# Optimization experiments

Measured on AMD Instinct MI355X. Metric: run time of the kernel, lower is better.

Reference implementation:

```python
import jax, jax.numpy as jnp
import numpy as np

N_NODES = 100000
N_EDGES = 3200000
STATE_DIM = 128
ACTION_DIM = 8


def _w(key, shape, scale=0.05):
    return (jax.random.normal(key, shape, dtype=jnp.float32) * scale)


def setup_inputs() -> dict:
    key = jax.random.key(0)
    ks = jax.random.split(key, 24)
    x = jax.random.normal(ks[0], (N_NODES, STATE_DIM), dtype=jnp.float32)
    edge_index = jax.random.randint(ks[1], (2, N_EDGES), 0, N_NODES, dtype=jnp.int64)
    inp = {
        "x": x,
        "edge_index": edge_index,
        # GCN layers (weights stored [in, out] so forward is x @ W + b)
        "W1": _w(ks[2], (STATE_DIM, 128)), "b1": jnp.zeros((128,), jnp.float32),
        "W2": _w(ks[3], (128, 128)),       "b2": jnp.zeros((128,), jnp.float32),
        "W3": _w(ks[4], (128, 64)),        "b3": jnp.zeros((64,), jnp.float32),
        # actor MLP 64->128->64->ACTION_DIM + softmax
        "Wa1": _w(ks[5], (64, 128)),  "ba1": jnp.zeros((128,), jnp.float32),
        "Wa2": _w(ks[6], (128, 64)),  "ba2": jnp.zeros((64,), jnp.float32),
        "Wa3": _w(ks[7], (64, ACTION_DIM)), "ba3": jnp.zeros((ACTION_DIM,), jnp.float32),
        # critic MLP 64->128->64->1
        "Wc1": _w(ks[8], (64, 128)),  "bc1": jnp.zeros((128,), jnp.float32),
        "Wc2": _w(ks[9], (128, 64)),  "bc2": jnp.zeros((64,), jnp.float32),
        "Wc3": _w(ks[10], (64, 1)),   "bc3": jnp.zeros((1,), jnp.float32),
    }
    return inp


def _gcn_conv(x, W, b, src, dst, norm):
    # GCNConv: D^{-1/2} (A + I) D^{-1/2} X W + b  (self loops already in src/dst)
    h = x @ W                                   # [N, out]
    msg = h[src] * norm[:, None]                # gather + per-edge scale
    agg = jax.ops.segment_sum(msg, dst, num_segments=N_NODES)
    return agg + b


def reference(x, edge_index,
              W1, b1, W2, b2, W3, b3,
              Wa1, ba1, Wa2, ba2, Wa3, ba3,
              Wc1, bc1, Wc2, bc2, Wc3, bc3):
    loop = jnp.arange(N_NODES, dtype=edge_index.dtype)
    src = jnp.concatenate([edge_index[0], loop])
    dst = jnp.concatenate([edge_index[1], loop])
    deg = jax.ops.segment_sum(jnp.ones_like(dst, dtype=x.dtype), dst,
                              num_segments=N_NODES)
    dinv = jax.lax.rsqrt(deg)                   # deg >= 1 via self loops
    norm = dinv[src] * dinv[dst]                # [E+N]

    # forward_gnn (dropout is identity in eval mode)
    h = jax.nn.relu(_gcn_conv(x, W1, b1, src, dst, norm))
    h = jax.nn.relu(_gcn_conv(h, W2, b2, src, dst, norm))
    h = _gcn_conv(h, W3, b3, src, dst, norm)    # [N, 64]

    a = jax.nn.relu(h @ Wa1 + ba1)
    a = jax.nn.relu(a @ Wa2 + ba2)
    probs = jax.nn.softmax(a @ Wa3 + ba3, axis=-1)   # [N, ACTION_DIM]

    c = jax.nn.relu(h @ Wc1 + bc1)
    c = jax.nn.relu(c @ Wc2 + bc2)
    values = c @ Wc3 + bc3                      # [N, 1]

    return jnp.concatenate([probs, values], axis=-1)  # [N, ACTION_DIM+1]
```

## Files before the change

kernel.cpp:

```cpp
#include <hip/hip_runtime.h>
#include <hip/hip_bf16.h>
#include <math.h>


#define WS_ALIGN(x) (((x) + 255) & ~(size_t)255)

constexpr int RNG  = 64;
constexpr int NRG  = 1563;
constexpr int NB   = 1024;
constexpr int CHK  = 16;

constexpr float S_FP8     = 64.0f;
constexpr float S_FP8_INV = 1.0f / 64.0f;

using bf16x8 = __attribute__((ext_vector_type(8))) short;
using f32x4  = __attribute__((ext_vector_type(4))) float;
using f32x2  = __attribute__((ext_vector_type(2))) float;

__device__ __forceinline__ float b2f(unsigned short u) {
    return __uint_as_float(((unsigned int)u) << 16);
}
__device__ __forceinline__ unsigned short f2b(float f) {
    __hip_bfloat16 hb = __float2bfloat16(f);
    return *(unsigned short*)&hb;
}
__device__ __forceinline__ unsigned char f2fp8(float f) {
    return (unsigned char)(__builtin_amdgcn_cvt_pk_fp8_f32(f, f, 0, false) & 0xff);
}
__device__ __forceinline__ int pad8(int v) { return (v + 7) & ~7; }

__device__ __forceinline__ void acc8(uint2 u, f32x2& a01, f32x2& a23,
                                     f32x2& a45, f32x2& a67) {
    a01 += __builtin_amdgcn_cvt_pk_f32_fp8((int)u.x, false);
    a23 += __builtin_amdgcn_cvt_pk_f32_fp8((int)u.x, true);
    a45 += __builtin_amdgcn_cvt_pk_f32_fp8((int)u.y, false);
    a67 += __builtin_amdgcn_cvt_pk_f32_fp8((int)u.y, true);
}


__global__ __launch_bounds__(256) void bucket_count_k(
    const int* __restrict__ dst, int* __restrict__ bcnt, int E) {
    __shared__ int c64[RNG];
    int b = blockIdx.x, t = threadIdx.x;
    if (t < RNG) c64[t] = 0;
    __syncthreads();
    int ec = (E + NB - 1) / NB;
    int e0 = b * ec, e1 = min(E, e0 + ec);
    for (int e = e0 + t; e < e1; e += 256) {
        int d = __builtin_nontemporal_load(dst + e);
        atomicAdd(&c64[d / NRG], 1);
    }
    __syncthreads();
    if (t < RNG) bcnt[t * NB + b] = c64[t];
}

__global__ __launch_bounds__(256) void rsum_k(
    const int* __restrict__ bcnt, int* __restrict__ base, int* __restrict__ rtot) {
    __shared__ int s[256];
    int r = blockIdx.x, t = threadIdx.x;
    const int* row = bcnt + (size_t)r * NB;
    int v[4], loc = 0;
#pragma unroll
    for (int j = 0; j < 4; j++) { v[j] = row[t * 4 + j]; loc += v[j]; }
    s[t] = loc;
    __syncthreads();
    for (int d = 1; d < 256; d <<= 1) {
        int x = (t >= d) ? s[t - d] : 0;
        __syncthreads();
        s[t] += x;
        __syncthreads();
    }
    int run = s[t] - loc;
    int* bp = base + (size_t)r * NB + t * 4;
#pragma unroll
    for (int j = 0; j < 4; j++) { bp[j] = run; run += v[j]; }
    if (t == 255) rtot[r] = s[255];
}

__global__ void rstart_k(const int* __restrict__ rtot, int* __restrict__ bstart, int E) {
    if (threadIdx.x == 0) {
        int run = 0;
        for (int r = 0; r < RNG; r++) { bstart[r] = run; run += rtot[r]; }
        bstart[RNG] = run;
    }
}

__global__ __launch_bounds__(256) void bucket_scatter_k(
    const int* __restrict__ src, const int* __restrict__ dst,
    const int* __restrict__ base, const int* __restrict__ bstart,
    unsigned* __restrict__ bucket, int E) {
    __shared__ int cur[RNG];
    int b = blockIdx.x, t = threadIdx.x;
    if (t < RNG) cur[t] = bstart[t] + base[(size_t)t * NB + b];
    __syncthreads();
    int ec = (E + NB - 1) / NB;
    int e0 = b * ec, e1 = min(E, e0 + ec);
    for (int e = e0 + t; e < e1; e += 256) {
        int d = __builtin_nontemporal_load(dst + e);
        int sv = __builtin_nontemporal_load(src + e);
        int r = d / NRG;
        int pos = atomicAdd(&cur[r], 1);
        bucket[pos] = ((unsigned)(d - r * NRG) << 17) | (unsigned)sv;
    }
}

__global__ __launch_bounds__(256) void hist_bucket_k(
    const unsigned* __restrict__ bucket, const int* __restrict__ bstart,
    int* __restrict__ hist) {
    __shared__ int h[NRG];
    int b = blockIdx.x, r = b & 63, c2 = b >> 6, t = threadIdx.x;
    for (int i = t; i < NRG; i += 256) h[i] = 0;
    int s0 = bstart[r], s1 = bstart[r + 1];
    int ec = (s1 - s0 + CHK - 1) / CHK;
    int e0 = s0 + c2 * ec, e1 = min(s1, e0 + ec);
    __syncthreads();
    for (int e = e0 + t; e < e1; e += 256) {
        unsigned v = __builtin_nontemporal_load(bucket + e);
        atomicAdd(&h[v >> 17], 1);
    }
    __syncthreads();
    int* out = hist + ((size_t)r * CHK + c2) * NRG;
    for (int i = t; i < NRG; i += 256) out[i] = h[i];
}

__global__ void sum_hist_dinv_k(const int* __restrict__ hist, int* __restrict__ cnt,
                                float* __restrict__ dinv, int N) {
    int i = blockIdx.x * 256 + threadIdx.x;
    if (i >= N) return;
    int r = i / NRG, li = i - r * NRG;
    const int* hp = hist + ((size_t)r * CHK) * NRG + li;
    int s = 0;
#pragma unroll
    for (int c = 0; c < CHK; c++) s += hp[(size_t)c * NRG];
    cnt[i] = s;
    dinv[i] = rsqrtf((float)s + 1.0f);
}

__global__ void chunk_sum_k(const int* __restrict__ cnt, int* __restrict__ bsum, int n) {
    __shared__ int sd[256];
    int t = threadIdx.x;
    int i = blockIdx.x * 256 + t;
    sd[t] = (i < n) ? pad8(cnt[i]) : 0;
    __syncthreads();
    for (int d = 128; d > 0; d >>= 1) {
        if (t < d) sd[t] += sd[t + d];
        __syncthreads();
    }
    if (t == 0) bsum[blockIdx.x] = sd[0];
}

__global__ void scan_mid_k(const int* __restrict__ bsum, int* __restrict__ boff,
                           int nb, int* __restrict__ rowptr, int N) {
    __shared__ int s[512];
    int t = threadIdx.x;
    s[t] = (t < nb) ? bsum[t] : 0;
    __syncthreads();
    if (t == 0) {
        int run = 0;
        for (int i = 0; i < nb; i++) { int v = s[i]; s[i] = run; run += v; }
        rowptr[N] = run;
    }
    __syncthreads();
    if (t < nb) boff[t] = s[t];
}

__global__ void scan_off_pad_k(const int* __restrict__ cnt, const int* __restrict__ boff,
                               int* __restrict__ rowptr, int* __restrict__ hist,
                               int* __restrict__ col, int N) {
    __shared__ int s[256];
    int t = threadIdx.x;
    int i = blockIdx.x * 256 + t;
    int cv = (i < N) ? cnt[i] : 0;
    int v = pad8(cv);
    if (i >= N) v = 0;
    s[t] = v;
    __syncthreads();
    for (int d = 1; d < 256; d <<= 1) {
        int x = (t >= d) ? s[t - d] : 0;
        __syncthreads();
        s[t] += x;
        __syncthreads();
    }
    if (i < N) {
        int rp = s[t] - v + boff[blockIdx.x];
        rowptr[i] = rp;
        int r = i / NRG, li = i - r * NRG;
        int* hp = hist + ((size_t)r * CHK) * NRG + li;
        int run = rp;
#pragma unroll
        for (int c = 0; c < CHK; c++) {
            int hv = hp[(size_t)c * NRG];
            hp[(size_t)c * NRG] = run;
            run += hv;
        }
        for (int e = rp + cv; e < rp + v; e++) col[e] = N;
    }
}

__global__ __launch_bounds__(256) void fill2_k(
    const unsigned* __restrict__ bucket, const int* __restrict__ bstart,
    const int* __restrict__ hist, int* __restrict__ col) {
    __shared__ int cur[NRG];
    int b = blockIdx.x, r = b & 63, c2 = b >> 6, t = threadIdx.x;
    const int* hp = hist + ((size_t)r * CHK + c2) * NRG;
    for (int i = t; i < NRG; i += 256) cur[i] = hp[i];
    int s0 = bstart[r], s1 = bstart[r + 1];
    int ec = (s1 - s0 + CHK - 1) / CHK;
    int e0 = s0 + c2 * ec, e1 = min(s1, e0 + ec);
    __syncthreads();
    for (int e = e0 + t; e < e1; e += 256) {
        unsigned v = __builtin_nontemporal_load(bucket + e);
        int slot = atomicAdd(&cur[v >> 17], 1);
        col[slot] = (int)(v & 0x1FFFFu);
    }
}


__global__ __launch_bounds__(256) void prep_w_k(
    const float* __restrict__ W1, const float* __restrict__ W2,
    const float* __restrict__ W3, const float* __restrict__ Wa1,
    const float* __restrict__ Wc1, const float* __restrict__ Wa2,
    const float* __restrict__ Wc2, unsigned short* __restrict__ wt) {
    int i = blockIdx.x * 256 + threadIdx.x;
    const float* W; int off, K, OUT;
    if (i < 16384)      { W = W1;  off = 0;     K = 128; OUT = 128; }
    else if (i < 32768) { W = W2;  off = 16384; K = 128; OUT = 128; }
    else if (i < 40960) { W = W3;  off = 32768; K = 128; OUT = 64; }
    else if (i < 49152) { W = Wa1; off = 40960; K = 64;  OUT = 128; }
    else if (i < 57344) { W = Wc1; off = 49152; K = 64;  OUT = 128; }
    else if (i < 65536) { W = Wa2; off = 57344; K = 128; OUT = 64; }
    else                { W = Wc2; off = 65536; K = 128; OUT = 64; }
    int j = i - off, k = j / OUT, n = j - k * OUT;
    wt[off + n * K + k] = f2b(W[j]);
}


template <int K, int OUT, int EPI, bool AF32>
__global__ __launch_bounds__(256) void gemm2_k(
    const void* __restrict__ Xv, int ldx, const unsigned short* __restrict__ Wt,
    const float* __restrict__ sb, const float* __restrict__ w3b,
    const float* __restrict__ b3, void* __restrict__ Yv, int N, int NT) {
    constexpr int LDK = K + 8;
    __shared__ __align__(16) unsigned short Bs[OUT * LDK];
    __shared__ __align__(16) unsigned short As[64 * LDK];
    int t = threadIdx.x;

    for (int g = t; g < OUT * (K / 8); g += 256) {
        int r = g / (K / 8), q = g - r * (K / 8);
        *(uint4*)&Bs[r * LDK + q * 8] = *(const uint4*)(Wt + r * K + q * 8);
    }

    int wv = t >> 6, lane = t & 63;
    int lm = lane & 15, lq = lane >> 4;
    constexpr int CT = OUT / 16;

    for (int tile = blockIdx.x; tile < NT; tile += gridDim.x) {
        int rowBase = tile * 64;

        if constexpr (AF32) {
            const float* X = (const float*)Xv;
            for (int g = t; g < 64 * (K / 8); g += 256) {
                int r = g / (K / 8), q = g - r * (K / 8);
                int gr = rowBase + r;
                unsigned short us[8];
                if (gr < N) {
                    float4 v0 = *(const float4*)(X + (size_t)gr * ldx + q * 8);
                    float4 v1 = *(const float4*)(X + (size_t)gr * ldx + q * 8 + 4);
                    us[0] = f2b(v0.x); us[1] = f2b(v0.y); us[2] = f2b(v0.z); us[3] = f2b(v0.w);
                    us[4] = f2b(v1.x); us[5] = f2b(v1.y); us[6] = f2b(v1.z); us[7] = f2b(v1.w);
                } else {
#pragma unroll
                    for (int j = 0; j < 8; j++) us[j] = 0;
                }
                *(uint4*)&As[r * LDK + q * 8] = *(uint4*)us;
            }
        } else {
            const unsigned short* X = (const unsigned short*)Xv;
            for (int g = t; g < 64 * (K / 8); g += 256) {
                int r = g / (K / 8), q = g - r * (K / 8);
                int gr = rowBase + r;
                uint4 v = make_uint4(0, 0, 0, 0);
                if (gr < N) v = *(const uint4*)(X + (size_t)gr * ldx + q * 8);
                *(uint4*)&As[r * LDK + q * 8] = v;
            }
        }
        __syncthreads();

        f32x4 acc[CT];
#pragma unroll
        for (int c = 0; c < CT; c++) acc[c] = (f32x4){0.f, 0.f, 0.f, 0.f};

        const unsigned short* arow = &As[(wv * 16 + lm) * LDK + lq * 8];
#pragma unroll
        for (int kt = 0; kt < K / 32; kt++) {
            bf16x8 a = *(const bf16x8*)(arow + kt * 32);
#pragma unroll
            for (int c = 0; c < CT; c++) {
                bf16x8 b = *(const bf16x8*)&Bs[(c * 16 + lm) * LDK + kt * 32 + lq * 8];
                acc[c] = __builtin_amdgcn_mfma_f32_16x16x32_bf16(a, b, acc[c], 0, 0, 0);
            }
        }

        int r0 = rowBase + wv * 16 + lq * 4;
        if constexpr (EPI == 0) {
#pragma unroll
            for (int r = 0; r < 4; r++) {
                int gr = r0 + r;
                float scale = (gr < N) ? sb[gr] * S_FP8 : 0.f;
#pragma unroll
                for (int c = 0; c < CT; c++) {
                    int colg = c * 16 + lm;
                    ((unsigned char*)Yv)[(size_t)gr * OUT + colg] = f2fp8(acc[c][r] * scale);
                }
            }
        }
        __syncthreads();
    }
}


template <bool RELU>
__global__ __launch_bounds__(256) void agg128_k(
    const unsigned char* __restrict__ H,
    const int* __restrict__ rowptr, const int* __restrict__ col,
    const float* __restrict__ dinv, const float* __restrict__ bias,
    unsigned short* __restrict__ Y, int N, int Ecap) {
    int tid = threadIdx.x;
    int node = blockIdx.x * 4 + (tid >> 6);
    if (node >= N) return;
    int lane = tid & 63;
    int grp = lane >> 4;
    int li8 = (lane & 15) * 8;

    f32x2 a01 = {0.f, 0.f}, a23 = {0.f, 0.f}, a45 = {0.f, 0.f}, a67 = {0.f, 0.f};
    if (grp == 0) {
        uint2 u = *(const uint2*)(H + (size_t)node * 128 + li8);
        acc8(u, a01, a23, a45, a67);
    }

    int start = rowptr[node], end = rowptr[node + 1];
    for (int e0 = start; e0 < end; e0 += 64) {
        int cv = col[min(e0 + lane, Ecap - 1)];
        int quads = min(64, end - e0) >> 2;
        for (int q = 0; q < quads; q += 2) {
            int s0 = __shfl(cv, 4 * q + grp, 64);
            int s1 = __shfl(cv, 4 * q + 4 + grp, 64);
            uint2 u0 = *(const uint2*)(H + (size_t)s0 * 128 + li8);
            uint2 u1 = *(const uint2*)(H + (size_t)s1 * 128 + li8);
            acc8(u0, a01, a23, a45, a67);
            acc8(u1, a01, a23, a45, a67);
        }
    }

#pragma unroll
    for (int w = 16; w < 64; w <<= 1) {
        a01[0] += __shfl_xor(a01[0], w, 64); a01[1] += __shfl_xor(a01[1], w, 64);
        a23[0] += __shfl_xor(a23[0], w, 64); a23[1] += __shfl_xor(a23[1], w, 64);
        a45[0] += __shfl_xor(a45[0], w, 64); a45[1] += __shfl_xor(a45[1], w, 64);
        a67[0] += __shfl_xor(a67[0], w, 64); a67[1] += __shfl_xor(a67[1], w, 64);
    }

    if (grp == 0) {
        float dv = dinv[node] * S_FP8_INV;
        float4 b0 = *(const float4*)(bias + li8);
        float4 b1 = *(const float4*)(bias + li8 + 4);
        float o0 = a01[0] * dv + b0.x, o1 = a01[1] * dv + b0.y;
        float o2 = a23[0] * dv + b0.z, o3 = a23[1] * dv + b0.w;
        float o4 = a45[0] * dv + b1.x, o5 = a45[1] * dv + b1.y;
        float o6 = a67[0] * dv + b1.z, o7 = a67[1] * dv + b1.w;
        if (RELU) {
            o0 = fmaxf(o0, 0.f); o1 = fmaxf(o1, 0.f); o2 = fmaxf(o2, 0.f); o3 = fmaxf(o3, 0.f);
            o4 = fmaxf(o4, 0.f); o5 = fmaxf(o5, 0.f); o6 = fmaxf(o6, 0.f); o7 = fmaxf(o7, 0.f);
        }
        unsigned short us[8] = {f2b(o0), f2b(o1), f2b(o2), f2b(o3),
                                f2b(o4), f2b(o5), f2b(o6), f2b(o7)};
        *(uint4*)(Y + (size_t)node * 128 + li8) = *(uint4*)us;
    }
}

__global__ __launch_bounds__(256) void agg64_k(
    const unsigned char* __restrict__ H,
    const int* __restrict__ rowptr, const int* __restrict__ col,
    const float* __restrict__ dinv, const float* __restrict__ bias,
    unsigned short* __restrict__ Y, int N, int Ecap) {
    int tid = threadIdx.x;
    int node = blockIdx.x * 4 + (tid >> 6);
    if (node >= N) return;
    int lane = tid & 63;
    int grp = lane >> 3;
    int li8 = (lane & 7) * 8;

    f32x2 a01 = {0.f, 0.f}, a23 = {0.f, 0.f}, a45 = {0.f, 0.f}, a67 = {0.f, 0.f};
    if (grp == 0) {
        uint2 u = *(const uint2*)(H + (size_t)node * 64 + li8);
        acc8(u, a01, a23, a45, a67);
    }

    int start = rowptr[node], end = rowptr[node + 1];
    for (int e0 = start; e0 < end; e0 += 64) {
        int cv = col[min(e0 + lane, Ecap - 1)];
        int octs = min(64, end - e0) >> 3;
        int o = 0;
        for (; o + 2 <= octs; o += 2) {
            int s0 = __shfl(cv, 8 * o + grp, 64);
            int s1 = __shfl(cv, 8 * o + 8 + grp, 64);
            uint2 u0 = *(const uint2*)(H + (size_t)s0 * 64 + li8);
            uint2 u1 = *(const uint2*)(H + (size_t)s1 * 64 + li8);
            acc8(u0, a01, a23, a45, a67);
            acc8(u1, a01, a23, a45, a67);
        }
        if (o < octs) {
            int s0 = __shfl(cv, 8 * o + grp, 64);
            uint2 u0 = *(const uint2*)(H + (size_t)s0 * 64 + li8);
            acc8(u0, a01, a23, a45, a67);
        }
    }

#pragma unroll
    for (int w = 8; w < 64; w <<= 1) {
        a01[0] += __shfl_xor(a01[0], w, 64); a01[1] += __shfl_xor(a01[1], w, 64);
        a23[0] += __shfl_xor(a23[0], w, 64); a23[1] += __shfl_xor(a23[1], w, 64);
        a45[0] += __shfl_xor(a45[0], w, 64); a45[1] += __shfl_xor(a45[1], w, 64);
        a67[0] += __shfl_xor(a67[0], w, 64); a67[1] += __shfl_xor(a67[1], w, 64);
    }

    if (grp == 0) {
        float dv = dinv[node] * S_FP8_INV;
        float4 b0 = *(const float4*)(bias + li8);
        float4 b1 = *(const float4*)(bias + li8 + 4);
        unsigned short us[8] = {
            f2b(a01[0] * dv + b0.x), f2b(a01[1] * dv + b0.y),
            f2b(a23[0] * dv + b0.z), f2b(a23[1] * dv + b0.w),
            f2b(a45[0] * dv + b1.x), f2b(a45[1] * dv + b1.y),
            f2b(a67[0] * dv + b1.z), f2b(a67[1] * dv + b1.w)};
        *(uint4*)(Y + (size_t)node * 64 + li8) = *(uint4*)us;
    }
}


template <int EPI>
__global__ __launch_bounds__(256) void heads_k(
    const unsigned short* __restrict__ h3,
    const unsigned short* __restrict__ W1t,
    const float* __restrict__ b1v,
    const unsigned short* __restrict__ W2t,
    const float* __restrict__ b2v,
    const float* __restrict__ w3,
    const float* __restrict__ b3v,
    float* __restrict__ out, int N, int NT) {
    constexpr int LD64 = 72, LD128 = 136;
    __shared__ __align__(16) unsigned short Bs1[128 * LD64];
    __shared__ __align__(16) unsigned short Bs2[64 * LD128];
    __shared__ __align__(16) unsigned short As[4 * 16 * LD64];
    __shared__ __align__(16) unsigned short A1[4 * 16 * LD128];
    int t = threadIdx.x, wv = t >> 6, lane = t & 63;
    int lm = lane & 15, lq = lane >> 4;

    for (int g = t; g < 128 * 8; g += 256) {
        int r = g >> 3, q = g & 7;
        *(uint4*)&Bs1[r * LD64 + q * 8] = *(const uint4*)(W1t + r * 64 + q * 8);
    }
    for (int g = t; g < 64 * 16; g += 256) {
        int r = g >> 4, q = g & 15;
        *(uint4*)&Bs2[r * LD128 + q * 8] = *(const uint4*)(W2t + r * 128 + q * 8);
    }
    __syncthreads();

    unsigned short* Asw = &As[wv * 16 * LD64];
    unsigned short* A1w = &A1[wv * 16 * LD128];

    for (int tile = blockIdx.x; tile < NT; tile += gridDim.x) {
        int rowBase = tile * 64 + wv * 16;

        for (int g = lane; g < 16 * 8; g += 64) {
            int r = g >> 3, q = g & 7;
            int gr = rowBase + r;
            uint4 v = make_uint4(0, 0, 0, 0);
            if (gr < N) v = *(const uint4*)(h3 + (size_t)gr * 64 + q * 8);
            *(uint4*)&Asw[r * LD64 + q * 8] = v;
        }

        f32x4 acc1[8];
#pragma unroll
        for (int c = 0; c < 8; c++) acc1[c] = (f32x4){0.f, 0.f, 0.f, 0.f};
        const unsigned short* arow = &Asw[lm * LD64 + lq * 8];
#pragma unroll
        for (int kt = 0; kt < 2; kt++) {
            bf16x8 a = *(const bf16x8*)(arow + kt * 32);
#pragma unroll
            for (int c = 0; c < 8; c++) {
                bf16x8 b = *(const bf16x8*)&Bs1[(c * 16 + lm) * LD64 + kt * 32 + lq * 8];
                acc1[c] = __builtin_amdgcn_mfma_f32_16x16x32_bf16(a, b, acc1[c], 0, 0, 0);
            }
        }
#pragma unroll
        for (int r = 0; r < 4; r++) {
            int lr = lq * 4 + r;
#pragma unroll
            for (int c = 0; c < 8; c++) {
                int colg = c * 16 + lm;
                float v = fmaxf(acc1[c][r] + b1v[colg], 0.f);
                A1w[lr * LD128 + colg] = f2b(v);
            }
        }

        f32x4 acc[4];
#pragma unroll
        for (int c = 0; c < 4; c++) acc[c] = (f32x4){0.f, 0.f, 0.f, 0.f};
        const unsigned short* arow2 = &A1w[lm * LD128 + lq * 8];
#pragma unroll
        for (int kt = 0; kt < 4; kt++) {
            bf16x8 a = *(const bf16x8*)(arow2 + kt * 32);
#pragma unroll
            for (int c = 0; c < 4; c++) {
                bf16x8 b = *(const bf16x8*)&Bs2[(c * 16 + lm) * LD128 + kt * 32 + lq * 8];
                acc[c] = __builtin_amdgcn_mfma_f32_16x16x32_bf16(a, b, acc[c], 0, 0, 0);
            }
        }

        int r0 = rowBase + lq * 4;
        if constexpr (EPI == 2) {
            float l[4][8];
#pragma unroll
            for (int r = 0; r < 4; r++)
#pragma unroll
                for (int a = 0; a < 8; a++) l[r][a] = 0.f;
#pragma unroll
            for (int c = 0; c < 4; c++) {
                int colg = c * 16 + lm;
#pragma unroll
                for (int r = 0; r < 4; r++) {
                    float v = fmaxf(acc[c][r] + b2v[colg], 0.f);
#pragma unroll
                    for (int a = 0; a < 8; a++)
                        l[r][a] = fmaf(v, w3[colg * 8 + a], l[r][a]);
                }
            }
#pragma unroll
            for (int w = 1; w < 16; w <<= 1)
#pragma unroll
                for (int r = 0; r < 4; r++)
#pragma unroll
                    for (int a = 0; a < 8; a++)
                        l[r][a] += __shfl_xor(l[r][a], w, 64);
            if (lm < 8) {
#pragma unroll
                for (int r = 0; r < 4; r++) {
                    int gr = r0 + r;
                    if (gr < N) {
                        float lg[8], m = -1e30f;
#pragma unroll
                        for (int a = 0; a < 8; a++) { lg[a] = l[r][a] + b3v[a]; m = fmaxf(m, lg[a]); }
                        float sum = 0.f;
#pragma unroll
                        for (int a = 0; a < 8; a++) { lg[a] = expf(lg[a] - m); sum += lg[a]; }
                        out[(size_t)gr * 9 + lm] = lg[lm] / sum;
                    }
                }
            }
        } else {
            float lv[4] = {0.f, 0.f, 0.f, 0.f};
#pragma unroll
            for (int c = 0; c < 4; c++) {
                int colg = c * 16 + lm;
#pragma unroll
                for (int r = 0; r < 4; r++) {
                    float v = fmaxf(acc[c][r] + b2v[colg], 0.f);
                    lv[r] = fmaf(v, w3[colg], lv[r]);
                }
            }
#pragma unroll
            for (int w = 1; w < 16; w <<= 1)
#pragma unroll
                for (int r = 0; r < 4; r++) lv[r] += __shfl_xor(lv[r], w, 64);
            if (lm == 0) {
#pragma unroll
                for (int r = 0; r < 4; r++) {
                    int gr = r0 + r;
                    if (gr < N) out[(size_t)gr * 9 + 8] = lv[r] + b3v[0];
                }
            }
        }
    }
}


extern "C" void kernel_launch(void* const* d_in, const int* in_sizes, int n_in,
                              void* d_out, int out_size, void* d_ws, size_t ws_size,
                              hipStream_t stream) {
    const float* x   = (const float*)d_in[0];
    const int*   ei  = (const int*)d_in[1];
    const float* W1  = (const float*)d_in[2];  const float* b1  = (const float*)d_in[3];
    const float* W2  = (const float*)d_in[4];  const float* b2  = (const float*)d_in[5];
    const float* W3  = (const float*)d_in[6];  const float* b3  = (const float*)d_in[7];
    const float* Wa1 = (const float*)d_in[8];  const float* ba1 = (const float*)d_in[9];
    const float* Wa2 = (const float*)d_in[10]; const float* ba2 = (const float*)d_in[11];
    const float* Wa3 = (const float*)d_in[12]; const float* ba3 = (const float*)d_in[13];
    const float* Wc1 = (const float*)d_in[14]; const float* bc1 = (const float*)d_in[15];
    const float* Wc2 = (const float*)d_in[16]; const float* bc2 = (const float*)d_in[17];
    const float* Wc3 = (const float*)d_in[18]; const float* bc3 = (const float*)d_in[19];
    float* out = (float*)d_out;

    const int N = in_sizes[0] / 128;
    const int E = in_sizes[1] / 2;
    const int* src = ei;
    const int* dst = ei + E;
    const int Ecap = E + 8 * N;
    const int Npad = ((N + 63) / 64) * 64;
    const int NT   = (N + 63) / 64;

    size_t off = 0;
    auto take = [&](size_t bytes) { size_t o = off; off = WS_ALIGN(off + bytes); return o; };
    char* ws = (char*)d_ws;
    unsigned short* h3     = (unsigned short*)(ws + take((size_t)N * 64 * 2));
    unsigned short* h      = (unsigned short*)(ws + take((size_t)N * 128 * 2));
    unsigned char*  hpr8   = (unsigned char*) (ws + take((size_t)(Npad + 64) * 128));
    int*            col    = (int*)(ws + take((size_t)Ecap * 4));
    unsigned short* wt     = (unsigned short*)(ws + take(73728 * 2));
    float* dinv   = (float*)(ws + take((size_t)(N + 64) * 4));
    int*   cnt    = (int*)  (ws + take((size_t)N * 4));
    int*   rowptr = (int*)  (ws + take((size_t)(N + 1) * 4));
    int*   bcnt   = (int*)  (ws + take((size_t)RNG * NB * 4));
    int*   base   = (int*)  (ws + take((size_t)RNG * NB * 4));
    int*   rtot   = (int*)  (ws + take(RNG * 4));
    int*   bstart = (int*)  (ws + take((RNG + 1) * 4));
    int*   bsum   = (int*)  (ws + take(512 * 4));
    int*   boff   = (int*)  (ws + take(512 * 4));
    unsigned* bucket = (unsigned*)h;
    int* hist = (int*)h3;
    (void)ws_size; (void)n_in; (void)out_size;

    const int nb  = (N + 255) / 256;
    const int gN  = (N + 255) / 256;
    const int GG  = 512;

    prep_w_k<<<288, 256, 0, stream>>>(W1, W2, W3, Wa1, Wc1, Wa2, Wc2, wt);
    const unsigned short* W1t  = wt;
    const unsigned short* W2t  = wt + 16384;
    const unsigned short* W3t  = wt + 32768;
    const unsigned short* Wh1t = wt + 40960;
    const unsigned short* Wa2t = wt + 57344;
    const unsigned short* Wc2t = wt + 65536;

    bucket_count_k<<<NB, 256, 0, stream>>>(dst, bcnt, E);
    rsum_k<<<RNG, 256, 0, stream>>>(bcnt, base, rtot);
    rstart_k<<<1, 64, 0, stream>>>(rtot, bstart, E);
    bucket_scatter_k<<<NB, 256, 0, stream>>>(src, dst, base, bstart, bucket, E);
    hist_bucket_k<<<RNG * CHK, 256, 0, stream>>>(bucket, bstart, hist);
    sum_hist_dinv_k<<<gN, 256, 0, stream>>>(hist, cnt, dinv, N);
    chunk_sum_k<<<nb, 256, 0, stream>>>(cnt, bsum, N);
    scan_mid_k<<<1, 512, 0, stream>>>(bsum, boff, nb, rowptr, N);
    scan_off_pad_k<<<nb, 256, 0, stream>>>(cnt, boff, rowptr, hist, col, N);
    fill2_k<<<RNG * CHK, 256, 0, stream>>>(bucket, bstart, hist, col);

    gemm2_k<128, 128, 0, true><<<GG, 256, 0, stream>>>(
        x, 128, W1t, dinv, nullptr, nullptr, hpr8, N, NT);
    agg128_k<true><<<(N + 3) / 4, 256, 0, stream>>>(hpr8, rowptr, col, dinv, b1, h, N, Ecap);
    gemm2_k<128, 128, 0, false><<<GG, 256, 0, stream>>>(
        h, 128, W2t, dinv, nullptr, nullptr, hpr8, N, NT);
    agg128_k<true><<<(N + 3) / 4, 256, 0, stream>>>(hpr8, rowptr, col, dinv, b2, h, N, Ecap);
    gemm2_k<128, 64, 0, false><<<GG, 256, 0, stream>>>(
        h, 128, W3t, dinv, nullptr, nullptr, hpr8, N, NT);
    agg64_k<<<(N + 3) / 4, 256, 0, stream>>>(hpr8, rowptr, col, dinv, b3, h3, N, Ecap);

    heads_k<2><<<GG, 256, 0, stream>>>(h3, Wh1t, ba1, Wa2t, ba2, Wa3, ba3, out, N, NT);
    heads_k<3><<<GG, 256, 0, stream>>>(h3, Wh1t + 128 * 64, bc1, Wc2t, bc2, Wc3, bc3, out, N, NT);
}
```

Before: 482.7 us.

## Fuse scan kernels, merge actor/critic heads, and retune GEMM grid sizes

Folds the chunk-sum into the degree/dinv kernel and replaces the single-block mid scan by having each scan block reduce the preceding block sums itself, removing two launches. The actor and critic head kernels are merged into one kernel that loads the h3 tile once, and it now reads weights directly from global memory instead of staging them in LDS. Grid sizes for the GEMM kernels and the heads kernel are raised. The tradeoffs are redundant prefix reductions over bsum in every scan block and uncached global weight reads in the heads kernel.

```diff
diff --git a/kernel.cpp b/kernel.cpp
--- a/kernel.cpp
+++ b/kernel.cpp
@@ -123,24 +123,22 @@
     for (int i = t; i < NRG; i += 256) out[i] = h[i];
 }
 
-__global__ void sum_hist_dinv_k(const int* __restrict__ hist, int* __restrict__ cnt,
-                                float* __restrict__ dinv, int N) {
-    int i = blockIdx.x * 256 + threadIdx.x;
-    if (i >= N) return;
-    int r = i / NRG, li = i - r * NRG;
-    const int* hp = hist + ((size_t)r * CHK) * NRG + li;
-    int s = 0;
-#pragma unroll
-    for (int c = 0; c < CHK; c++) s += hp[(size_t)c * NRG];
-    cnt[i] = s;
-    dinv[i] = rsqrtf((float)s + 1.0f);
-}
-
-__global__ void chunk_sum_k(const int* __restrict__ cnt, int* __restrict__ bsum, int n) {
+__global__ __launch_bounds__(256) void sum_hist_dinv_k(
+    const int* __restrict__ hist, int* __restrict__ cnt,
+    float* __restrict__ dinv, int* __restrict__ bsum, int N) {
     __shared__ int sd[256];
     int t = threadIdx.x;
     int i = blockIdx.x * 256 + t;
-    sd[t] = (i < n) ? pad8(cnt[i]) : 0;
+    int s = 0;
+    if (i < N) {
+        int r = i / NRG, li = i - r * NRG;
+        const int* hp = hist + ((size_t)r * CHK) * NRG + li;
+#pragma unroll
+        for (int c = 0; c < CHK; c++) s += hp[(size_t)c * NRG];
+        cnt[i] = s;
+        dinv[i] = rsqrtf((float)s + 1.0f);
+    }
+    sd[t] = (i < N) ? pad8(s) : 0;
     __syncthreads();
     for (int d = 128; d > 0; d >>= 1) {
         if (t < d) sd[t] += sd[t + d];
@@ -149,27 +147,24 @@
     if (t == 0) bsum[blockIdx.x] = sd[0];
 }
 
-__global__ void scan_mid_k(const int* __restrict__ bsum, int* __restrict__ boff,
-                           int nb, int* __restrict__ rowptr, int N) {
-    __shared__ int s[512];
-    int t = threadIdx.x;
-    s[t] = (t < nb) ? bsum[t] : 0;
-    __syncthreads();
-    if (t == 0) {
-        int run = 0;
-        for (int i = 0; i < nb; i++) { int v = s[i]; s[i] = run; run += v; }
-        rowptr[N] = run;
-    }
-    __syncthreads();
-    if (t < nb) boff[t] = s[t];
-}
-
-__global__ void scan_off_pad_k(const int* __restrict__ cnt, const int* __restrict__ boff,
+__global__ void scan_off_pad_k(const int* __restrict__ cnt, const int* __restrict__ bsum,
                                int* __restrict__ rowptr, int* __restrict__ hist,
                                int* __restrict__ col, int N) {
     __shared__ int s[256];
-    int t = threadIdx.x;
-    int i = blockIdx.x * 256 + t;
+    int t = threadIdx.x, b = blockIdx.x;
+
+    int part = 0;
+    for (int j = t; j < b; j += 256) part += bsum[j];
+    s[t] = part;
+    __syncthreads();
+    for (int d = 128; d > 0; d >>= 1) {
+        if (t < d) s[t] += s[t + d];
+        __syncthreads();
+    }
+    int boffv = s[0];
+    __syncthreads();
+
+    int i = b * 256 + t;
     int cv = (i < N) ? cnt[i] : 0;
     int v = pad8(cv);
     if (i >= N) v = 0;
@@ -181,8 +176,9 @@
         s[t] += x;
         __syncthreads();
     }
+    if (b == (int)gridDim.x - 1 && t == 255) rowptr[N] = boffv + s[255];
     if (i < N) {
-        int rp = s[t] - v + boff[blockIdx.x];
+        int rp = s[t] - v + boffv;
         rowptr[i] = rp;
         int r = i / NRG, li = i - r * NRG;
         int* hp = hist + ((size_t)r * CHK) * NRG + li;
@@ -438,34 +434,22 @@
 }
 
 
-template <int EPI>
-__global__ __launch_bounds__(256) void heads_k(
+__global__ __launch_bounds__(256) void headsAC_k(
     const unsigned short* __restrict__ h3,
-    const unsigned short* __restrict__ W1t,
-    const float* __restrict__ b1v,
-    const unsigned short* __restrict__ W2t,
-    const float* __restrict__ b2v,
-    const float* __restrict__ w3,
-    const float* __restrict__ b3v,
+    const unsigned short* __restrict__ Wh1t,
+    const float* __restrict__ ba1, const float* __restrict__ bc1,
+    const unsigned short* __restrict__ Wa2t,
+    const float* __restrict__ ba2,
+    const unsigned short* __restrict__ Wc2t,
+    const float* __restrict__ bc2,
+    const float* __restrict__ Wa3, const float* __restrict__ ba3,
+    const float* __restrict__ Wc3, const float* __restrict__ bc3,
     float* __restrict__ out, int N, int NT) {
     constexpr int LD64 = 72, LD128 = 136;
-    __shared__ __align__(16) unsigned short Bs1[128 * LD64];
-    __shared__ __align__(16) unsigned short Bs2[64 * LD128];
     __shared__ __align__(16) unsigned short As[4 * 16 * LD64];
     __shared__ __align__(16) unsigned short A1[4 * 16 * LD128];
     int t = threadIdx.x, wv = t >> 6, lane = t & 63;
     int lm = lane & 15, lq = lane >> 4;
-
-    for (int g = t; g < 128 * 8; g += 256) {
-        int r = g >> 3, q = g & 7;
-        *(uint4*)&Bs1[r * LD64 + q * 8] = *(const uint4*)(W1t + r * 64 + q * 8);
-    }
-    for (int g = t; g < 64 * 16; g += 256) {
-        int r = g >> 4, q = g & 15;
-        *(uint4*)&Bs2[r * LD128 + q * 8] = *(const uint4*)(W2t + r * 128 + q * 8);
-    }
-    __syncthreads();
-
     unsigned short* Asw = &As[wv * 16 * LD64];
     unsigned short* A1w = &A1[wv * 16 * LD128];
 
@@ -479,47 +463,47 @@
             if (gr < N) v = *(const uint4*)(h3 + (size_t)gr * 64 + q * 8);
             *(uint4*)&Asw[r * LD64 + q * 8] = v;
         }
-
-        f32x4 acc1[8];
-#pragma unroll
-        for (int c = 0; c < 8; c++) acc1[c] = (f32x4){0.f, 0.f, 0.f, 0.f};
         const unsigned short* arow = &Asw[lm * LD64 + lq * 8];
-#pragma unroll
-        for (int kt = 0; kt < 2; kt++) {
-            bf16x8 a = *(const bf16x8*)(arow + kt * 32);
-#pragma unroll
-            for (int c = 0; c < 8; c++) {
-                bf16x8 b = *(const bf16x8*)&Bs1[(c * 16 + lm) * LD64 + kt * 32 + lq * 8];
-                acc1[c] = __builtin_amdgcn_mfma_f32_16x16x32_bf16(a, b, acc1[c], 0, 0, 0);
-            }
-        }
-#pragma unroll
-        for (int r = 0; r < 4; r++) {
-            int lr = lq * 4 + r;
-#pragma unroll
-            for (int c = 0; c < 8; c++) {
-                int colg = c * 16 + lm;
-                float v = fmaxf(acc1[c][r] + b1v[colg], 0.f);
-                A1w[lr * LD128 + colg] = f2b(v);
-            }
-        }
-
-        f32x4 acc[4];
-#pragma unroll
-        for (int c = 0; c < 4; c++) acc[c] = (f32x4){0.f, 0.f, 0.f, 0.f};
-        const unsigned short* arow2 = &A1w[lm * LD128 + lq * 8];
-#pragma unroll
-        for (int kt = 0; kt < 4; kt++) {
-            bf16x8 a = *(const bf16x8*)(arow2 + kt * 32);
-#pragma unroll
-            for (int c = 0; c < 4; c++) {
-                bf16x8 b = *(const bf16x8*)&Bs2[(c * 16 + lm) * LD128 + kt * 32 + lq * 8];
-                acc[c] = __builtin_amdgcn_mfma_f32_16x16x32_bf16(a, b, acc[c], 0, 0, 0);
-            }
-        }
-
         int r0 = rowBase + lq * 4;
-        if constexpr (EPI == 2) {
+
+        {
+            f32x4 acc1[8];
+#pragma unroll
+            for (int c = 0; c < 8; c++) acc1[c] = (f32x4){0.f, 0.f, 0.f, 0.f};
+#pragma unroll
+            for (int kt = 0; kt < 2; kt++) {
+                bf16x8 a = *(const bf16x8*)(arow + kt * 32);
+#pragma unroll
+                for (int c = 0; c < 8; c++) {
+                    bf16x8 b = *(const bf16x8*)(Wh1t + (size_t)(c * 16 + lm) * 64 + kt * 32 + lq * 8);
+                    acc1[c] = __builtin_amdgcn_mfma_f32_16x16x32_bf16(a, b, acc1[c], 0, 0, 0);
+                }
+            }
+#pragma unroll
+            for (int r = 0; r < 4; r++) {
+                int lr = lq * 4 + r;
+#pragma unroll
+                for (int c = 0; c < 8; c++) {
+                    int colg = c * 16 + lm;
+                    float v = fmaxf(acc1[c][r] + ba1[colg], 0.f);
+                    A1w[lr * LD128 + colg] = f2b(v);
+                }
+            }
+
+            f32x4 acc[4];
+#pragma unroll
+            for (int c = 0; c < 4; c++) acc[c] = (f32x4){0.f, 0.f, 0.f, 0.f};
+            const unsigned short* arow2 = &A1w[lm * LD128 + lq * 8];
+#pragma unroll
+            for (int kt = 0; kt < 4; kt++) {
+                bf16x8 a = *(const bf16x8*)(arow2 + kt * 32);
+#pragma unroll
+                for (int c = 0; c < 4; c++) {
+                    bf16x8 b = *(const bf16x8*)(Wa2t + (size_t)(c * 16 + lm) * 128 + kt * 32 + lq * 8);
+                    acc[c] = __builtin_amdgcn_mfma_f32_16x16x32_bf16(a, b, acc[c], 0, 0, 0);
+                }
+            }
+
             float l[4][8];
 #pragma unroll
             for (int r = 0; r < 4; r++)
@@ -530,10 +514,10 @@
                 int colg = c * 16 + lm;
 #pragma unroll
                 for (int r = 0; r < 4; r++) {
-                    float v = fmaxf(acc[c][r] + b2v[colg], 0.f);
+                    float v = fmaxf(acc[c][r] + ba2[colg], 0.f);
 #pragma unroll
                     for (int a = 0; a < 8; a++)
-                        l[r][a] = fmaf(v, w3[colg * 8 + a], l[r][a]);
+                        l[r][a] = fmaf(v, Wa3[colg * 8 + a], l[r][a]);
                 }
             }
 #pragma unroll
@@ -550,7 +534,7 @@
                     if (gr < N) {
                         float lg[8], m = -1e30f;
 #pragma unroll
-                        for (int a = 0; a < 8; a++) { lg[a] = l[r][a] + b3v[a]; m = fmaxf(m, lg[a]); }
+                        for (int a = 0; a < 8; a++) { lg[a] = l[r][a] + ba3[a]; m = fmaxf(m, lg[a]); }
                         float sum = 0.f;
 #pragma unroll
                         for (int a = 0; a < 8; a++) { lg[a] = expf(lg[a] - m); sum += lg[a]; }
@@ -558,15 +542,54 @@
                     }
                 }
             }
-        } else {
+        }
+
+        {
+            f32x4 acc1[8];
+#pragma unroll
+            for (int c = 0; c < 8; c++) acc1[c] = (f32x4){0.f, 0.f, 0.f, 0.f};
+#pragma unroll
+            for (int kt = 0; kt < 2; kt++) {
+                bf16x8 a = *(const bf16x8*)(arow + kt * 32);
+#pragma unroll
+                for (int c = 0; c < 8; c++) {
+                    bf16x8 b = *(const bf16x8*)(Wh1t + (size_t)(128 + c * 16 + lm) * 64 + kt * 32 + lq * 8);
+                    acc1[c] = __builtin_amdgcn_mfma_f32_16x16x32_bf16(a, b, acc1[c], 0, 0, 0);
+                }
+            }
+#pragma unroll
+            for (int r = 0; r < 4; r++) {
+                int lr = lq * 4 + r;
+#pragma unroll
+                for (int c = 0; c < 8; c++) {
+                    int colg = c * 16 + lm;
+                    float v = fmaxf(acc1[c][r] + bc1[colg], 0.f);
+                    A1w[lr * LD128 + colg] = f2b(v);
+                }
+            }
+
+            f32x4 acc[4];
+#pragma unroll
+            for (int c = 0; c < 4; c++) acc[c] = (f32x4){0.f, 0.f, 0.f, 0.f};
+            const unsigned short* arow2 = &A1w[lm * LD128 + lq * 8];
+#pragma unroll
+            for (int kt = 0; kt < 4; kt++) {
+                bf16x8 a = *(const bf16x8*)(arow2 + kt * 32);
+#pragma unroll
+                for (int c = 0; c < 4; c++) {
+                    bf16x8 b = *(const bf16x8*)(Wc2t + (size_t)(c * 16 + lm) * 128 + kt * 32 + lq * 8);
+                    acc[c] = __builtin_amdgcn_mfma_f32_16x16x32_bf16(a, b, acc[c], 0, 0, 0);
+                }
+            }
+
             float lv[4] = {0.f, 0.f, 0.f, 0.f};
 #pragma unroll
             for (int c = 0; c < 4; c++) {
                 int colg = c * 16 + lm;
 #pragma unroll
                 for (int r = 0; r < 4; r++) {
-                    float v = fmaxf(acc[c][r] + b2v[colg], 0.f);
-                    lv[r] = fmaf(v, w3[colg], lv[r]);
+                    float v = fmaxf(acc[c][r] + bc2[colg], 0.f);
+                    lv[r] = fmaf(v, Wc3[colg], lv[r]);
                 }
             }
 #pragma unroll
@@ -577,7 +600,7 @@
 #pragma unroll
                 for (int r = 0; r < 4; r++) {
                     int gr = r0 + r;
-                    if (gr < N) out[(size_t)gr * 9 + 8] = lv[r] + b3v[0];
+                    if (gr < N) out[(size_t)gr * 9 + 8] = lv[r] + bc3[0];
                 }
             }
         }
@@ -625,14 +648,13 @@
     int*   rtot   = (int*)  (ws + take(RNG * 4));
     int*   bstart = (int*)  (ws + take((RNG + 1) * 4));
     int*   bsum   = (int*)  (ws + take(512 * 4));
-    int*   boff   = (int*)  (ws + take(512 * 4));
     unsigned* bucket = (unsigned*)h;
     int* hist = (int*)h3;
     (void)ws_size; (void)n_in; (void)out_size;
 
     const int nb  = (N + 255) / 256;
-    const int gN  = (N + 255) / 256;
-    const int GG  = 512;
+    const int GG128 = 768;
+    const int GG64  = 1024;
 
     prep_w_k<<<288, 256, 0, stream>>>(W1, W2, W3, Wa1, Wc1, Wa2, Wc2, wt);
     const unsigned short* W1t  = wt;
@@ -647,22 +669,20 @@
     rstart_k<<<1, 64, 0, stream>>>(rtot, bstart, E);
     bucket_scatter_k<<<NB, 256, 0, stream>>>(src, dst, base, bstart, bucket, E);
     hist_bucket_k<<<RNG * CHK, 256, 0, stream>>>(bucket, bstart, hist);
-    sum_hist_dinv_k<<<gN, 256, 0, stream>>>(hist, cnt, dinv, N);
-    chunk_sum_k<<<nb, 256, 0, stream>>>(cnt, bsum, N);
-    scan_mid_k<<<1, 512, 0, stream>>>(bsum, boff, nb, rowptr, N);
-    scan_off_pad_k<<<nb, 256, 0, stream>>>(cnt, boff, rowptr, hist, col, N);
+    sum_hist_dinv_k<<<nb, 256, 0, stream>>>(hist, cnt, dinv, bsum, N);
+    scan_off_pad_k<<<nb, 256, 0, stream>>>(cnt, bsum, rowptr, hist, col, N);
     fill2_k<<<RNG * CHK, 256, 0, stream>>>(bucket, bstart, hist, col);
 
-    gemm2_k<128, 128, 0, true><<<GG, 256, 0, stream>>>(
+    gemm2_k<128, 128, 0, true><<<GG128, 256, 0, stream>>>(
         x, 128, W1t, dinv, nullptr, nullptr, hpr8, N, NT);
     agg128_k<true><<<(N + 3) / 4, 256, 0, stream>>>(hpr8, rowptr, col, dinv, b1, h, N, Ecap);
-    gemm2_k<128, 128, 0, false><<<GG, 256, 0, stream>>>(
+    gemm2_k<128, 128, 0, false><<<GG128, 256, 0, stream>>>(
         h, 128, W2t, dinv, nullptr, nullptr, hpr8, N, NT);
     agg128_k<true><<<(N + 3) / 4, 256, 0, stream>>>(hpr8, rowptr, col, dinv, b2, h, N, Ecap);
-    gemm2_k<128, 64, 0, false><<<GG, 256, 0, stream>>>(
+    gemm2_k<128, 64, 0, false><<<GG64, 256, 0, stream>>>(
         h, 128, W3t, dinv, nullptr, nullptr, hpr8, N, NT);
     agg64_k<<<(N + 3) / 4, 256, 0, stream>>>(hpr8, rowptr, col, dinv, b3, h3, N, Ecap);
 
-    heads_k<2><<<GG, 256, 0, stream>>>(h3, Wh1t, ba1, Wa2t, ba2, Wa3, ba3, out, N, NT);
-    heads_k<3><<<GG, 256, 0, stream>>>(h3, Wh1t + 128 * 64, bc1, Wc2t, bc2, Wc3, bc3, out, N, NT);
-}
+    headsAC_k<<<1024, 256, 0, stream>>>(
+        h3, Wh1t, ba1, bc1, Wa2t, ba2, Wc2t, bc2, Wa3, ba3, Wc3, bc3, out, N, NT);
+}
```

Result: slower. 507.9 us (+5.2%).
